# Kernel optimization log

Measured on AMD Instinct MI355X. Metric: run time of the kernel, lower is better.

## Reference

```python
import jax, jax.numpy as jnp
import numpy as np

DX, DZ, DT = 10.0, 10.0, 1.0e-3
NX, NZ = 512, 512
NSTEPS, NREC = 512, 128
DT2 = DT * DT
INV_DXDZ = 1.0 / (DX * DZ)


def setup_inputs() -> dict:
    key = jax.random.key(0)
    k1, k2, k3, k4 = jax.random.split(key, 4)
    # velocity in [1500, 2500] m/s -> CFL stable with dt=1e-3, dx=dz=10
    velocity_model = 1500.0 + 1000.0 * jax.random.uniform(k1, (NX, NZ), dtype=jnp.float32)
    source = jax.random.normal(k2, (NSTEPS,), dtype=jnp.float32)
    rec_x = jax.random.randint(k3, (NREC,), 0, NX)
    rec_z = jax.random.randint(k4, (NREC,), 0, NZ)
    return {
        "velocity_model": velocity_model,
        "source": source,
        "src_x": 256,
        "src_z": 8,
        "rec_x": rec_x,
        "rec_z": rec_z,
    }


def _laplacian(p):
    # 3x3 cross stencil with zero padding, scaled by 1/(dx*dz) -- identical to
    # F.conv2d(p, [[0,1,0],[1,-4,1],[0,1,0]]/(dx*dz), padding=1)
    pp = jnp.pad(p, 1)
    return (pp[:-2, 1:-1] + pp[2:, 1:-1] + pp[1:-1, :-2] + pp[1:-1, 2:] - 4.0 * p) * INV_DXDZ


def reference(velocity_model, source, src_x, src_z, rec_x, rec_z):
    v2_dt2 = velocity_model * velocity_model * DT2  # [nx, nz]

    def step(carry, s_t):
        p, p_old = carry
        p_new = 2.0 * p - p_old + v2_dt2 * _laplacian(p)
        p_new = p_new.at[src_x, src_z].add(s_t * DT2)
        return (p_new, p), p_new[rec_x, rec_z]  # gather all receivers at once

    p0 = jnp.zeros((NX, NZ), dtype=velocity_model.dtype)
    _, recs = jax.lax.scan(step, (p0, p0), source)  # recs: [n_steps, n_rec]
    return recs.T  # seismogram: [n_rec, n_steps]
```

## Files before the change

### kernel.cpp

```cpp
#include <hip/hip_runtime.h>


#define NXd 512
#define NZd 512
#define NSTEPSd 512
#define NRECd 128
#define DT2f 1.0e-6f
#define INVf 1.0e-2f
#define TBk 16
#define TIk 32
#define EXTk 64
#define NTILEk 16

__device__ __forceinline__ float dpp_shr1(float x) {
    int v = __builtin_amdgcn_update_dpp(0, __builtin_bit_cast(int, x),
                                        0x138, 0xF, 0xF, false);
    return __builtin_bit_cast(float, v);
}
__device__ __forceinline__ float dpp_shl1(float x) {
    int v = __builtin_amdgcn_update_dpp(0, __builtin_bit_cast(int, x),
                                        0x130, 0xF, 0xF, false);
    return __builtin_bit_cast(float, v);
}

__global__ __launch_bounds__(1024) void fdtd_tblock(
    const float* __restrict__ vel,
    const float* __restrict__ source,
    const int* __restrict__ src_x, const int* __restrict__ src_z,
    const int* __restrict__ rec_x, const int* __restrict__ rec_z,
    const float* __restrict__ Gc_in, const float* __restrict__ Go_in,
    float* __restrict__ Gc_out, float* __restrict__ Go_out,
    float* __restrict__ out, int t0)
{
    __shared__ float sb[2][EXTk * EXTk];

    const int tid = threadIdx.x;
    const int w   = tid >> 6;
    const int ez  = tid & 63;
    const int gx0 = blockIdx.y * TIk, gz0 = blockIdx.x * TIk;
    const int ox = gx0 - TBk, oz = gz0 - TBk;

    const int sx = *src_x, sz = *src_z;

    bool rOwn = false; int rIdx = 0;
    if (tid < NRECd) {
        int rx = rec_x[tid], rz = rec_z[tid];
        rOwn = (rx >= gx0 && rx < gx0 + TIk && rz >= gz0 && rz < gz0 + TIk);
        rIdx = (rx - gx0 + TBk) * EXTk + (rz - gz0 + TBk);
    }

    {
        int dxm = max(0, max(ox - sx, sx - (ox + EXTk - 1)));
        int dzm = max(0, max(oz - sz, sz - (oz + EXTk - 1)));
        if (dxm + dzm > t0 + TBk + 1) {
            if (rOwn) {
                #pragma unroll
                for (int s = 0; s < TBk; ++s)
                    out[tid * NSTEPSd + t0 + s] = 0.0f;
            }
            return;
        }
    }

    const int gz = oz + ez;
    const bool zin = (gz >= 0 && gz < NZd);
    float rCur[4], rOld[4], rV2i[4];
    #pragma unroll
    for (int i = 0; i < 4; ++i) {
        const int ex = 4 * w + i;
        const int gx = ox + ex;
        float c = 0.0f, o = 0.0f, v2 = 0.0f;
        if (zin && gx >= 0 && gx < NXd) {
            const int g = gx * NZd + gz;
            c = Gc_in[g];
            o = Go_in[g];
            const float v = vel[g];
            v2 = v * v * (DT2f * INVf);
        }
        rCur[i] = c; rOld[i] = o; rV2i[i] = v2;
        sb[0][ex * EXTk + ez] = c;
    }
    const int rowUp = (w == 0)  ? 0             : 4 * w - 1;
    const int rowDn = (w == 15) ? EXTk - 1      : 4 * w + 4;

    const int exs = sx - ox, ezs = sz - oz;
    const bool srcHere = (exs >= 0 && exs < EXTk && ezs >= 0 && ezs < EXTk) &&
                         (tid == (((exs >> 2) << 6) | ezs));
    float sv[TBk];
    if (srcHere) {
        #pragma unroll
        for (int s = 0; s < TBk; ++s) sv[s] = source[t0 + s] * DT2f;
    }

    __syncthreads();

    #pragma unroll
    for (int s = 0; s < TBk; ++s) {
        const float* cur = sb[s & 1];
        float* nxt = sb[(s & 1) ^ 1];
        const float up0 = cur[rowUp * EXTk + ez];
        const float dn3 = cur[rowDn * EXTk + ez];
        float nv[4];
        #pragma unroll
        for (int i = 0; i < 4; ++i) {
            const float up = (i == 0) ? up0 : rCur[i - 1];
            const float dn = (i == 3) ? dn3 : rCur[i + 1];
            const float lf = dpp_shr1(rCur[i]);
            const float rt = dpp_shl1(rCur[i]);
            const float sum = (up + dn) + (lf + rt);
            const float t4 = __builtin_fmaf(-4.0f, rCur[i], sum);
            const float pm = __builtin_fmaf(2.0f, rCur[i], -rOld[i]);
            nv[i] = __builtin_fmaf(rV2i[i], t4, pm);
        }
        #pragma unroll
        for (int i = 0; i < 4; ++i) {
            rOld[i] = rCur[i];
            rCur[i] = nv[i];
            nxt[(4 * w + i) * EXTk + ez] = nv[i];
        }
        if (srcHere) {
            #pragma unroll
            for (int i = 0; i < 4; ++i) {
                if (i == (exs & 3)) {
                    rCur[i] += sv[s];
                    nxt[exs * EXTk + ezs] = rCur[i];
                }
            }
        }
        __syncthreads();
        if (rOwn) out[tid * NSTEPSd + t0 + s] = nxt[rIdx];
    }

    if (w >= 4 && w < 12 && ez >= TBk && ez < EXTk - TBk) {
        #pragma unroll
        for (int i = 0; i < 4; ++i) {
            const int g = (ox + 4 * w + i) * NZd + gz;
            Gc_out[g] = rCur[i];
            Go_out[g] = rOld[i];
        }
    }
}

extern "C" void kernel_launch(void* const* d_in, const int* in_sizes, int n_in,
                              void* d_out, int out_size, void* d_ws, size_t ws_size,
                              hipStream_t stream) {
    const float* vel    = (const float*)d_in[0];
    const float* source = (const float*)d_in[1];
    const int*   src_x  = (const int*)d_in[2];
    const int*   src_z  = (const int*)d_in[3];
    const int*   rec_x  = (const int*)d_in[4];
    const int*   rec_z  = (const int*)d_in[5];
    float* out = (float*)d_out;

    const size_t F = (size_t)NXd * NZd;
    float* A_c = (float*)d_ws;
    float* A_o = A_c + F;
    float* B_c = A_o + F;
    float* B_o = B_c + F;

    hipMemsetAsync(d_ws, 0, 4 * F * sizeof(float), stream);

    dim3 grid(NTILEk, NTILEk), block(1024);
    for (int k = 0; k < NSTEPSd / TBk; ++k) {
        const float *ic, *io; float *oc, *oo;
        if (k & 1) { ic = B_c; io = B_o; oc = A_c; oo = A_o; }
        else       { ic = A_c; io = A_o; oc = B_c; oo = B_o; }
        fdtd_tblock<<<grid, block, 0, stream>>>(vel, source, src_x, src_z,
                                                rec_x, rec_z, ic, io, oc, oo,
                                                out, k * TBk);
    }
}
```

Measured before the change: 374.1 us.

## Replace per-phase kernel launches with persistent cooperative kernel using neighbor flags

```diff
diff --git a/kernel.cpp b/kernel.cpp
--- a/kernel.cpp
+++ b/kernel.cpp
@@ -11,6 +11,8 @@
 #define TIk 32
 #define EXTk 64
 #define NTILEk 16
+#define NPHASEk 32
+#define ROWSk 16
 
 __device__ __forceinline__ float dpp_shr1(float x) {
     int v = __builtin_amdgcn_update_dpp(0, __builtin_bit_cast(int, x),
@@ -23,120 +25,195 @@
     return __builtin_bit_cast(float, v);
 }
 
-__global__ __launch_bounds__(1024) void fdtd_tblock(
-    const float* __restrict__ vel,
-    const float* __restrict__ source,
+__global__ __launch_bounds__(256, 1) void fdtd_persist(
+    const float* __restrict__ vel, const float* __restrict__ source,
     const int* __restrict__ src_x, const int* __restrict__ src_z,
     const int* __restrict__ rec_x, const int* __restrict__ rec_z,
-    const float* __restrict__ Gc_in, const float* __restrict__ Go_in,
-    float* __restrict__ Gc_out, float* __restrict__ Go_out,
-    float* __restrict__ out, int t0)
+    float* __restrict__ Ca, float* __restrict__ Oa,
+    float* __restrict__ Cb, float* __restrict__ Ob,
+    int* __restrict__ ctrs, float* __restrict__ out)
 {
-    __shared__ float sb[2][EXTk * EXTk];
+    __shared__ float sb[2][8 * EXTk];
+    __shared__ float recLDS[2][EXTk * EXTk];
 
     const int tid = threadIdx.x;
-    const int w   = tid >> 6;
-    const int ez  = tid & 63;
-    const int gx0 = blockIdx.y * TIk, gz0 = blockIdx.x * TIk;
+    const int w = tid >> 6;
+    const int lane = tid & 63;
+    const int bx = blockIdx.y, bz = blockIdx.x;
+    const int gx0 = bx * TIk, gz0 = bz * TIk;
     const int ox = gx0 - TBk, oz = gz0 - TBk;
-
+    const int gz = oz + lane;
+    const bool zin = (gz >= 0 && gz < NZd);
     const int sx = *src_x, sz = *src_z;
+    const int myb = bx * NTILEk + bz;
+
+    float rV2i[ROWSk];
+    #pragma unroll
+    for (int i = 0; i < ROWSk; ++i) {
+        int gx = ox + ROWSk * w + i;
+        float v2 = 0.f;
+        if (zin && gx >= 0 && gx < NXd) {
+            float v = vel[gx * NZd + gz];
+            v2 = v * v * (DT2f * INVf);
+        }
+        rV2i[i] = v2;
+    }
 
     bool rOwn = false; int rIdx = 0;
     if (tid < NRECd) {
         int rx = rec_x[tid], rz = rec_z[tid];
-        rOwn = (rx >= gx0 && rx < gx0 + TIk && rz >= gz0 && rz < gz0 + TIk);
-        rIdx = (rx - gx0 + TBk) * EXTk + (rz - gz0 + TBk);
-    }
-
-    {
+        if (rx >= gx0 && rx < gx0 + TIk && rz >= gz0 && rz < gz0 + TIk) {
+            rOwn = true;
+            rIdx = (rx - ox) * EXTk + (rz - oz);
+        }
+    }
+    bool anyRec = false;
+    unsigned ownMask = 0;
+    for (int j = 0; j < NRECd; ++j) {
+        int rx = rec_x[j], rz = rec_z[j];
+        if (rx >= gx0 && rx < gx0 + TIk && rz >= gz0 && rz < gz0 + TIk) {
+            anyRec = true;
+            int exr = rx - ox, exc = rz - oz;
+            if ((exr >> 4) == w && exc == lane) ownMask |= 1u << (exr & 15);
+        }
+    }
+
+    const int exs = sx - ox, ezs = sz - oz;
+    const bool srcHere = exs >= 0 && exs < EXTk && ezs >= 0 && ezs < EXTk &&
+                         w == (exs >> 4) && lane == ezs;
+    const int srcI = exs & 15;
+
+    if ((w == 1 || w == 2) && lane >= TBk && lane < EXTk - TBk) {
+        #pragma unroll
+        for (int i = 0; i < ROWSk; ++i) {
+            int g = (ox + ROWSk * w + i) * NZd + gz;
+            Ca[g] = 0.f; Oa[g] = 0.f; Cb[g] = 0.f; Ob[g] = 0.f;
+        }
+    }
+    __syncthreads();
+    if (tid == 0) {
+        __threadfence();
+        __hip_atomic_store(&ctrs[myb], 1, __ATOMIC_RELEASE,
+                           __HIP_MEMORY_SCOPE_AGENT);
+    }
+
+    int nbIdx = -1;
+    if (tid < 8) {
+        const int dxs[8] = {-1,-1,-1, 0, 0, 1, 1, 1};
+        const int dzs[8] = {-1, 0, 1,-1, 1,-1, 0, 1};
+        int nx = bx + dxs[tid], nz = bz + dzs[tid];
+        if (nx >= 0 && nx < NTILEk && nz >= 0 && nz < NTILEk)
+            nbIdx = nx * NTILEk + nz;
+    }
+
+    for (int p = 0; p < NPHASEk; ++p) {
+        const int t0 = p * TBk;
+
         int dxm = max(0, max(ox - sx, sx - (ox + EXTk - 1)));
         int dzm = max(0, max(oz - sz, sz - (oz + EXTk - 1)));
         if (dxm + dzm > t0 + TBk + 1) {
             if (rOwn) {
                 #pragma unroll
                 for (int s = 0; s < TBk; ++s)
-                    out[tid * NSTEPSd + t0 + s] = 0.0f;
-            }
-            return;
-        }
-    }
-
-    const int gz = oz + ez;
-    const bool zin = (gz >= 0 && gz < NZd);
-    float rCur[4], rOld[4], rV2i[4];
-    #pragma unroll
-    for (int i = 0; i < 4; ++i) {
-        const int ex = 4 * w + i;
-        const int gx = ox + ex;
-        float c = 0.0f, o = 0.0f, v2 = 0.0f;
-        if (zin && gx >= 0 && gx < NXd) {
-            const int g = gx * NZd + gz;
-            c = Gc_in[g];
-            o = Go_in[g];
-            const float v = vel[g];
-            v2 = v * v * (DT2f * INVf);
-        }
-        rCur[i] = c; rOld[i] = o; rV2i[i] = v2;
-        sb[0][ex * EXTk + ez] = c;
-    }
-    const int rowUp = (w == 0)  ? 0             : 4 * w - 1;
-    const int rowDn = (w == 15) ? EXTk - 1      : 4 * w + 4;
-
-    const int exs = sx - ox, ezs = sz - oz;
-    const bool srcHere = (exs >= 0 && exs < EXTk && ezs >= 0 && ezs < EXTk) &&
-                         (tid == (((exs >> 2) << 6) | ezs));
-    float sv[TBk];
-    if (srcHere) {
+                    out[tid * NSTEPSd + t0 + s] = 0.f;
+            }
+            __syncthreads();
+            if (tid == 0)
+                __hip_atomic_store(&ctrs[myb], p + 2, __ATOMIC_RELEASE,
+                                   __HIP_MEMORY_SCOPE_AGENT);
+            continue;
+        }
+
+        if (nbIdx >= 0) {
+            while (__hip_atomic_load(&ctrs[nbIdx], __ATOMIC_ACQUIRE,
+                                     __HIP_MEMORY_SCOPE_AGENT) < p + 1)
+                __builtin_amdgcn_s_sleep(1);
+        }
+        __syncthreads();
+
+        const float* Cin = (p & 1) ? Cb : Ca;
+        const float* Oin = (p & 1) ? Ob : Oa;
+        float* Cout = (p & 1) ? Ca : Cb;
+        float* Oout = (p & 1) ? Oa : Ob;
+
+        float rCur[ROWSk], rOld[ROWSk];
         #pragma unroll
-        for (int s = 0; s < TBk; ++s) sv[s] = source[t0 + s] * DT2f;
-    }
-
-    __syncthreads();
-
-    #pragma unroll
-    for (int s = 0; s < TBk; ++s) {
-        const float* cur = sb[s & 1];
-        float* nxt = sb[(s & 1) ^ 1];
-        const float up0 = cur[rowUp * EXTk + ez];
-        const float dn3 = cur[rowDn * EXTk + ez];
-        float nv[4];
+        for (int i = 0; i < ROWSk; ++i) {
+            int gx = ox + ROWSk * w + i;
+            float c = 0.f, o = 0.f;
+            if (zin && gx >= 0 && gx < NXd) {
+                int g = gx * NZd + gz;
+                c = Cin[g]; o = Oin[g];
+            }
+            rCur[i] = c; rOld[i] = o;
+        }
+
+        float sv[TBk];
+        if (srcHere) {
+            #pragma unroll
+            for (int s = 0; s < TBk; ++s) sv[s] = source[t0 + s] * DT2f;
+        }
+
+        sb[0][(2 * w) * EXTk + lane] = rCur[0];
+        sb[0][(2 * w + 1) * EXTk + lane] = rCur[ROWSk - 1];
+        __syncthreads();
+
+        float rv[TBk];
         #pragma unroll
-        for (int i = 0; i < 4; ++i) {
-            const float up = (i == 0) ? up0 : rCur[i - 1];
-            const float dn = (i == 3) ? dn3 : rCur[i + 1];
-            const float lf = dpp_shr1(rCur[i]);
-            const float rt = dpp_shl1(rCur[i]);
-            const float sum = (up + dn) + (lf + rt);
-            const float t4 = __builtin_fmaf(-4.0f, rCur[i], sum);
-            const float pm = __builtin_fmaf(2.0f, rCur[i], -rOld[i]);
-            nv[i] = __builtin_fmaf(rV2i[i], t4, pm);
-        }
-        #pragma unroll
-        for (int i = 0; i < 4; ++i) {
-            rOld[i] = rCur[i];
-            rCur[i] = nv[i];
-            nxt[(4 * w + i) * EXTk + ez] = nv[i];
-        }
-        if (srcHere) {
-            #pragma unroll
-            for (int i = 0; i < 4; ++i) {
-                if (i == (exs & 3)) {
-                    rCur[i] += sv[s];
-                    nxt[exs * EXTk + ezs] = rCur[i];
-                }
+        for (int s = 0; s < TBk; ++s) {
+            const float* cbuf = sb[s & 1];
+            float* nbuf = sb[(s & 1) ^ 1];
+            float up0 = (w > 0) ? cbuf[(2 * w - 1) * EXTk + lane] : 0.f;
+            float dn15 = (w < 3) ? cbuf[(2 * w + 2) * EXTk + lane] : 0.f;
+            float prev = up0;
+            #pragma unroll
+            for (int i = 0; i < ROWSk; ++i) {
+                float dnv = (i < ROWSk - 1) ? rCur[i + 1] : dn15;
+                float lf = dpp_shr1(rCur[i]);
+                float rt = dpp_shl1(rCur[i]);
+                float sum = (prev + dnv) + (lf + rt);
+                float t4 = __builtin_fmaf(-4.f, rCur[i], sum);
+                float pm = __builtin_fmaf(2.f, rCur[i], -rOld[i]);
+                float nv = __builtin_fmaf(rV2i[i], t4, pm);
+                prev = rCur[i];
+                rOld[i] = rCur[i];
+                rCur[i] = nv;
+            }
+            if (srcHere) {
+                #pragma unroll
+                for (int i = 0; i < ROWSk; ++i)
+                    if (i == srcI) rCur[i] += sv[s];
+            }
+            nbuf[(2 * w) * EXTk + lane] = rCur[0];
+            nbuf[(2 * w + 1) * EXTk + lane] = rCur[ROWSk - 1];
+            if (anyRec && ownMask) {
+                #pragma unroll
+                for (int i = 0; i < ROWSk; ++i)
+                    if (ownMask & (1u << i))
+                        recLDS[s & 1][(ROWSk * w + i) * EXTk + lane] = rCur[i];
+            }
+            __syncthreads();
+            if (rOwn) rv[s] = recLDS[s & 1][rIdx];
+        }
+
+        if (rOwn) {
+            #pragma unroll
+            for (int s = 0; s < TBk; ++s)
+                out[tid * NSTEPSd + t0 + s] = rv[s];
+        }
+        if ((w == 1 || w == 2) && lane >= TBk && lane < EXTk - TBk) {
+            #pragma unroll
+            for (int i = 0; i < ROWSk; ++i) {
+                int g = (ox + ROWSk * w + i) * NZd + gz;
+                Cout[g] = rCur[i];
+                Oout[g] = rOld[i];
             }
         }
         __syncthreads();
-        if (rOwn) out[tid * NSTEPSd + t0 + s] = nxt[rIdx];
-    }
-
-    if (w >= 4 && w < 12 && ez >= TBk && ez < EXTk - TBk) {
-        #pragma unroll
-        for (int i = 0; i < 4; ++i) {
-            const int g = (ox + 4 * w + i) * NZd + gz;
-            Gc_out[g] = rCur[i];
-            Go_out[g] = rOld[i];
+        if (tid == 0) {
+            __threadfence();
+            __hip_atomic_store(&ctrs[myb], p + 2, __ATOMIC_RELEASE,
+                               __HIP_MEMORY_SCOPE_AGENT);
         }
     }
 }
@@ -153,20 +230,17 @@
     float* out = (float*)d_out;
 
     const size_t F = (size_t)NXd * NZd;
-    float* A_c = (float*)d_ws;
-    float* A_o = A_c + F;
-    float* B_c = A_o + F;
-    float* B_o = B_c + F;
-
-    hipMemsetAsync(d_ws, 0, 4 * F * sizeof(float), stream);
-
-    dim3 grid(NTILEk, NTILEk), block(1024);
-    for (int k = 0; k < NSTEPSd / TBk; ++k) {
-        const float *ic, *io; float *oc, *oo;
-        if (k & 1) { ic = B_c; io = B_o; oc = A_c; oo = A_o; }
-        else       { ic = A_c; io = A_o; oc = B_c; oo = B_o; }
-        fdtd_tblock<<<grid, block, 0, stream>>>(vel, source, src_x, src_z,
-                                                rec_x, rec_z, ic, io, oc, oo,
-                                                out, k * TBk);
-    }
-}
+    float* Ca = (float*)d_ws;
+    float* Oa = Ca + F;
+    float* Cb = Oa + F;
+    float* Ob = Cb + F;
+    int* ctrs = (int*)(Ob + F);
+
+    hipMemsetAsync(ctrs, 0, NTILEk * NTILEk * sizeof(int), stream);
+
+    void* args[] = {(void*)&vel, (void*)&source, (void*)&src_x, (void*)&src_z,
+                    (void*)&rec_x, (void*)&rec_z, (void*)&Ca, (void*)&Oa,
+                    (void*)&Cb, (void*)&Ob, (void*)&ctrs, (void*)&out};
+    hipLaunchCooperativeKernel((void*)fdtd_persist, dim3(NTILEk, NTILEk),
+                               dim3(256), args, 0, stream);
+}
```

New measurement: 853.0 us. 128% more time.

## Interleave field pairs, shrink shared halo exchange, register-buffer receiver samples

Applied to the files above, without the earlier changes.

```diff
diff --git a/kernel.cpp b/kernel.cpp
--- a/kernel.cpp
+++ b/kernel.cpp
@@ -23,69 +23,81 @@
     return __builtin_bit_cast(float, v);
 }
 
+__device__ __forceinline__ float upd(float c, float o, float v2,
+                                     float up, float dn) {
+    float lf = dpp_shr1(c);
+    float rt = dpp_shl1(c);
+    float sum = (up + dn) + (lf + rt);
+    float t4 = __builtin_fmaf(-4.0f, c, sum);
+    float pm = __builtin_fmaf(2.0f, c, -o);
+    return __builtin_fmaf(v2, t4, pm);
+}
+
 __global__ __launch_bounds__(1024) void fdtd_tblock(
     const float* __restrict__ vel,
     const float* __restrict__ source,
     const int* __restrict__ src_x, const int* __restrict__ src_z,
     const int* __restrict__ rec_x, const int* __restrict__ rec_z,
-    const float* __restrict__ Gc_in, const float* __restrict__ Go_in,
-    float* __restrict__ Gc_out, float* __restrict__ Go_out,
+    const float2* __restrict__ Pin, float2* __restrict__ Pout,
     float* __restrict__ out, int t0)
 {
-    __shared__ float sb[2][EXTk * EXTk];
+    __shared__ float sb[2][32 * EXTk];
 
     const int tid = threadIdx.x;
-    const int w   = tid >> 6;
-    const int ez  = tid & 63;
+    const int w = tid >> 6;
+    const int lane = tid & 63;
     const int gx0 = blockIdx.y * TIk, gz0 = blockIdx.x * TIk;
     const int ox = gx0 - TBk, oz = gz0 - TBk;
-
+    const int gz = oz + lane;
+    const bool zin = (gz >= 0 && gz < NZd);
     const int sx = *src_x, sz = *src_z;
 
-    bool rOwn = false; int rIdx = 0;
-    if (tid < NRECd) {
-        int rx = rec_x[tid], rz = rec_z[tid];
-        rOwn = (rx >= gx0 && rx < gx0 + TIk && rz >= gz0 && rz < gz0 + TIk);
-        rIdx = (rx - gx0 + TBk) * EXTk + (rz - gz0 + TBk);
+    int s0rec = -1, s0i = 0;
+    int dcnt = 0, dRec[2], dIdx[2];
+    for (int j = 0; j < NRECd; ++j) {
+        int rx = rec_x[j], rz = rec_z[j];
+        if (rx >= gx0 && rx < gx0 + TIk && rz >= gz0 && rz < gz0 + TIk) {
+            int exr = rx - ox, exc = rz - oz;
+            if ((exr >> 2) == w && exc == lane) {
+                if (s0rec < 0) { s0rec = j; s0i = exr & 3; }
+                else if (dcnt < 2) { dRec[dcnt] = j; dIdx[dcnt] = exr & 3; ++dcnt; }
+            }
+        }
     }
 
     {
         int dxm = max(0, max(ox - sx, sx - (ox + EXTk - 1)));
         int dzm = max(0, max(oz - sz, sz - (oz + EXTk - 1)));
         if (dxm + dzm > t0 + TBk + 1) {
-            if (rOwn) {
-                #pragma unroll
-                for (int s = 0; s < TBk; ++s)
-                    out[tid * NSTEPSd + t0 + s] = 0.0f;
-            }
+            if (s0rec >= 0)
+                for (int s = 0; s < TBk; ++s) out[s0rec * NSTEPSd + t0 + s] = 0.f;
+            for (int k = 0; k < dcnt; ++k)
+                for (int s = 0; s < TBk; ++s) out[dRec[k] * NSTEPSd + t0 + s] = 0.f;
             return;
         }
     }
 
-    const int gz = oz + ez;
-    const bool zin = (gz >= 0 && gz < NZd);
-    float rCur[4], rOld[4], rV2i[4];
+    float rCur[4], rOld[4], rV2[4];
     #pragma unroll
     for (int i = 0; i < 4; ++i) {
-        const int ex = 4 * w + i;
-        const int gx = ox + ex;
-        float c = 0.0f, o = 0.0f, v2 = 0.0f;
+        const int gx = ox + 4 * w + i;
+        float c = 0.f, o = 0.f, v2 = 0.f;
         if (zin && gx >= 0 && gx < NXd) {
             const int g = gx * NZd + gz;
-            c = Gc_in[g];
-            o = Go_in[g];
-            const float v = vel[g];
+            float2 co = Pin[g];
+            c = co.x; o = co.y;
+            float v = vel[g];
             v2 = v * v * (DT2f * INVf);
         }
-        rCur[i] = c; rOld[i] = o; rV2i[i] = v2;
-        sb[0][ex * EXTk + ez] = c;
+        rCur[i] = c; rOld[i] = o; rV2[i] = v2;
     }
-    const int rowUp = (w == 0)  ? 0             : 4 * w - 1;
-    const int rowDn = (w == 15) ? EXTk - 1      : 4 * w + 4;
+    sb[0][(2 * w) * EXTk + lane] = rCur[0];
+    sb[0][(2 * w + 1) * EXTk + lane] = rCur[3];
 
     const int exs = sx - ox, ezs = sz - oz;
-    const bool srcHere = (exs >= 0 && exs < EXTk && ezs >= 0 && ezs < EXTk) &&
-                         (tid == (((exs >> 2) << 6) | ezs));
+    const bool srcHere = exs >= 0 && exs < EXTk && ezs >= 0 && ezs < EXTk &&
+                         w == (exs >> 2) && lane == ezs;
+    const int srcI = exs & 3;
     float sv[TBk];
     if (srcHere) {
         #pragma unroll
@@ -94,49 +106,51 @@
 
     __syncthreads();
 
+    float rv[8];
     #pragma unroll
     for (int s = 0; s < TBk; ++s) {
-        const float* cur = sb[s & 1];
-        float* nxt = sb[(s & 1) ^ 1];
-        const float up0 = cur[rowUp * EXTk + ez];
-        const float dn3 = cur[rowDn * EXTk + ez];
-        float nv[4];
-        #pragma unroll
-        for (int i = 0; i < 4; ++i) {
-            const float up = (i == 0) ? up0 : rCur[i - 1];
-            const float dn = (i == 3) ? dn3 : rCur[i + 1];
-            const float lf = dpp_shr1(rCur[i]);
-            const float rt = dpp_shl1(rCur[i]);
-            const float sum = (up + dn) + (lf + rt);
-            const float t4 = __builtin_fmaf(-4.0f, rCur[i], sum);
-            const float pm = __builtin_fmaf(2.0f, rCur[i], -rOld[i]);
-            nv[i] = __builtin_fmaf(rV2i[i], t4, pm);
+        const float* cb = sb[s & 1];
+        float* nb = sb[(s & 1) ^ 1];
+        const float up0 = (w > 0)  ? cb[(2 * w - 1) * EXTk + lane] : 0.f;
+        const float dn3 = (w < 15) ? cb[(2 * w + 2) * EXTk + lane] : 0.f;
+        float nv1 = upd(rCur[1], rOld[1], rV2[1], rCur[0], rCur[2]);
+        float nv2 = upd(rCur[2], rOld[2], rV2[2], rCur[1], rCur[3]);
+        float nv0 = upd(rCur[0], rOld[0], rV2[0], up0, rCur[1]);
+        float nv3 = upd(rCur[3], rOld[3], rV2[3], rCur[2], dn3);
+        if (srcHere) {
+            if (srcI == 0) nv0 += sv[s];
+            else if (srcI == 1) nv1 += sv[s];
+            else if (srcI == 2) nv2 += sv[s];
+            else nv3 += sv[s];
         }
-        #pragma unroll
-        for (int i = 0; i < 4; ++i) {
-            rOld[i] = rCur[i];
-            rCur[i] = nv[i];
-            nxt[(4 * w + i) * EXTk + ez] = nv[i];
-        }
-        if (srcHere) {
-            #pragma unroll
-            for (int i = 0; i < 4; ++i) {
-                if (i == (exs & 3)) {
-                    rCur[i] += sv[s];
-                    nxt[exs * EXTk + ezs] = rCur[i];
-                }
-            }
+        rOld[0] = rCur[0]; rCur[0] = nv0;
+        rOld[1] = rCur[1]; rCur[1] = nv1;
+        rOld[2] = rCur[2]; rCur[2] = nv2;
+        rOld[3] = rCur[3]; rCur[3] = nv3;
+        nb[(2 * w) * EXTk + lane] = nv0;
+        nb[(2 * w + 1) * EXTk + lane] = nv3;
+        if (s0rec >= 0)
+            rv[s & 7] = (s0i == 0) ? rCur[0] : (s0i == 1) ? rCur[1]
+                       : (s0i == 2) ? rCur[2] : rCur[3];
+        if (dcnt) {
+            for (int k = 0; k < dcnt; ++k)
+                out[dRec[k] * NSTEPSd + t0 + s] =
+                    (dIdx[k] == 0) ? rCur[0] : (dIdx[k] == 1) ? rCur[1]
+                   : (dIdx[k] == 2) ? rCur[2] : rCur[3];
         }
         __syncthreads();
-        if (rOwn) out[tid * NSTEPSd + t0 + s] = nxt[rIdx];
+        if ((s == 7 || s == 15) && s0rec >= 0) {
+            #pragma unroll
+            for (int q = 0; q < 8; ++q)
+                out[s0rec * NSTEPSd + t0 + (s - 7) + q] = rv[q];
+        }
     }
 
-    if (w >= 4 && w < 12 && ez >= TBk && ez < EXTk - TBk) {
+    if (w >= 4 && w < 12 && lane >= TBk && lane < EXTk - TBk) {
         #pragma unroll
         for (int i = 0; i < 4; ++i) {
             const int g = (ox + 4 * w + i) * NZd + gz;
-            Gc_out[g] = rCur[i];
-            Go_out[g] = rOld[i];
+            Pout[g] = make_float2(rCur[i], rOld[i]);
         }
     }
 }
@@ -153,20 +167,17 @@
     float* out = (float*)d_out;
 
     const size_t F = (size_t)NXd * NZd;
-    float* A_c = (float*)d_ws;
-    float* A_o = A_c + F;
-    float* B_c = A_o + F;
-    float* B_o = B_c + F;
+    float2* PA = (float2*)d_ws;
+    float2* PB = PA + F;
 
-    hipMemsetAsync(d_ws, 0, 4 * F * sizeof(float), stream);
+    hipMemsetAsync(d_ws, 0, 2 * F * sizeof(float2), stream);
 
     dim3 grid(NTILEk, NTILEk), block(1024);
     for (int k = 0; k < NSTEPSd / TBk; ++k) {
-        const float *ic, *io; float *oc, *oo;
-        if (k & 1) { ic = B_c; io = B_o; oc = A_c; oo = A_o; }
-        else       { ic = A_c; io = A_o; oc = B_c; oo = B_o; }
+        const float2* Pin = (k & 1) ? PB : PA;
+        float2* Pout      = (k & 1) ? PA : PB;
         fdtd_tblock<<<grid, block, 0, stream>>>(vel, source, src_x, src_z,
-                                                rec_x, rec_z, ic, io, oc, oo,
+                                                rec_x, rec_z, Pin, Pout,
                                                 out, k * TBk);
     }
 }
```

Result: slower. 952.8 us (+154.7%).
